# Optimization experiments

Measured on AMD Instinct MI355X. Metric: run time of the kernel, lower is better.

## Reference

```python
import jax, jax.numpy as jnp
import numpy as np


def _disk_samples(size):
    # Same construction as the torch module: regular grid on [-1,1]^2, keep points in unit disk.
    xs, ys = [], []
    for i in range(size):
        for j in range(size):
            x = i * 2.0 / (size - 1) - 1.0
            y = j * 2.0 / (size - 1) - 1.0
            if x * x + y * y <= 1.0:
                xs.append(x)
                ys.append(y)
    return np.asarray(xs, np.float32), np.asarray(ys, np.float32)


def setup_inputs() -> dict:
    key = jax.random.key(0)
    k1, k2, k3, k4, k5 = jax.random.split(key, 5)
    B, L, C, H, W = 1, 12, 3, 640, 640
    images = jax.random.uniform(k1, (B, L, C, H, W), dtype=jnp.float32)
    alphas = jax.random.uniform(k2, (B, L, 1, H, W), dtype=jnp.float32)
    coffs = jax.random.uniform(k3, (B, L, 1, H, W), dtype=jnp.float32)  # per-plane disparity-like map in [0,1)
    K = jax.random.uniform(k4, (B, 1, 1, 1), dtype=jnp.float32) * 20.0 + 2.0  # aperture radius in pixels
    depth_focus = jax.random.uniform(k5, (B, 1, 1, 1), dtype=jnp.float32)  # focus value, same units as coffs
    return {"images": images, "alphas": alphas, "coffs": coffs, "K": K,
            "depth_focus": depth_focus, "samples_per_side": 5}


def reference(images, alphas, coffs, K, depth_focus, samples_per_side):
    # Depth-aware ray-traced bokeh over an MPI stack.
    # For each output pixel and each circular aperture sample (u,v), gather from each
    # plane at an offset proportional to the plane's signed defocus radius
    #   r = K * (coff - depth_focus)
    # (nearest-pixel gather, clamped), then composite planes front-to-back with alpha,
    # and average over aperture samples.
    B, L, C, H, W = images.shape
    xs_np, ys_np = _disk_samples(int(samples_per_side))
    n_samples = len(xs_np)

    Kb = K[:, 0, 0, 0]                      # [B]
    df = depth_focus[:, 0, 0, 0]            # [B]
    coff = coffs[:, :, 0]                   # [B,L,H,W]
    r = Kb[:, None, None, None] * (coff - df[:, None, None, None])  # signed radius per plane/pixel

    a_flat = alphas[:, :, 0].reshape(B, L, H * W)       # [B,L,HW]
    img_flat = images.reshape(B, L, C, H * W)           # [B,L,C,HW]
    yy, xx = jnp.meshgrid(jnp.arange(H, dtype=jnp.float32),
                          jnp.arange(W, dtype=jnp.float32), indexing="ij")

    acc = jnp.zeros((B, C, H, W), images.dtype)
    for s in range(n_samples):  # small fixed aperture-sample set (static)
        qx = jnp.clip(jnp.round(xx + xs_np[s] * r), 0, W - 1).astype(jnp.int32)
        qy = jnp.clip(jnp.round(yy + ys_np[s] * r), 0, H - 1).astype(jnp.int32)
        idx = (qy * W + qx).reshape(B, L, H * W)
        a = jnp.take_along_axis(a_flat, idx, axis=2)                 # [B,L,HW]
        c = jnp.take_along_axis(img_flat, idx[:, :, None, :], axis=3)  # [B,L,C,HW]
        trans = jnp.cumprod(1.0 - a, axis=1)
        excl = jnp.concatenate([jnp.ones_like(a[:, :1]), trans[:, :-1]], axis=1)
        w = a * excl                                                  # front-to-back weights
        acc = acc + (w[:, :, None, :] * c).sum(axis=1).reshape(B, C, H, W)
    return acc / jnp.float32(n_samples)
```

## Files before the change

kernel.cpp:

```cpp
#include <hip/hip_runtime.h>

#define L_ 12
#define C_ 3
#define H_ 640
#define W_ 640
#define HW_ (H_*W_)

#define TS 40
#define HALO 22
#define LD (TS + 2*HALO)
#define NSLOT (LD*LD)
#define NT 1024
#define SIZE 5
#define NSAMP 13

__global__ __launch_bounds__(1024, 4) void render_tiled(
    const float* __restrict__ images,
    const float* __restrict__ alphas,
    const float* __restrict__ coffs,
    const float* __restrict__ Kp,
    const float* __restrict__ dfp,
    float* __restrict__ out) {
  __shared__ float4 tile[NSLOT];

  const int tid = threadIdx.x;
  const int tx0 = (int)(blockIdx.x % (W_ / TS)) * TS;
  const int ty0 = (int)(blockIdx.x / (W_ / TS)) * TS;
  const int bx0 = tx0 - HALO;
  const int by0 = ty0 - HALO;

  const float Kv = Kp[0];
  const float df = dfp[0];

  const int p0 = tid;
  const bool has2 = (tid < TS * TS - NT);
  const int p1 = tid + NT;

  const int x0 = tx0 + (p0 % TS), y0 = ty0 + (p0 / TS);
  const int x1 = tx0 + (p1 % TS), y1 = ty0 + (p1 / TS);
  const float xf0 = (float)x0, yf0 = (float)y0;
  const float xf1 = (float)x1, yf1 = (float)y1;

  float T0[NSAMP], T1[NSAMP];
#pragma unroll
  for (int s = 0; s < NSAMP; ++s) { T0[s] = 1.f; T1[s] = 1.f; }
  float a00 = 0.f, a01 = 0.f, a02 = 0.f;
  float a10 = 0.f, a11 = 0.f, a12 = 0.f;

  for (int l = 0; l < L_; ++l) {
    __syncthreads();
    const float* __restrict__ aP  = alphas + (size_t)l * HW_;
    const float* __restrict__ c0P = images + (size_t)(l * 3 + 0) * HW_;
    const float* __restrict__ c1P = images + (size_t)(l * 3 + 1) * HW_;
    const float* __restrict__ c2P = images + (size_t)(l * 3 + 2) * HW_;
    for (int s = tid; s < NSLOT; s += NT) {
      int hy = s / LD, hx = s - hy * LD;
      int gy = min(max(by0 + hy, 0), H_ - 1);
      int gx = min(max(bx0 + hx, 0), W_ - 1);
      int g = gy * W_ + gx;
      tile[s] = make_float4(aP[g], c0P[g], c1P[g], c2P[g]);
    }
    __syncthreads();

    const float r0 = __fmul_rn(Kv, __fsub_rn(coffs[(size_t)l * HW_ + y0 * W_ + x0], df));
    const float r1 = has2 ? __fmul_rn(Kv, __fsub_rn(coffs[(size_t)l * HW_ + y1 * W_ + x1], df)) : 0.f;

    int ord = 0;
#pragma unroll
    for (int i = 0; i < SIZE; ++i) {
#pragma unroll
      for (int j = 0; j < SIZE; ++j) {
        const double dx = (double)i * 2.0 / (SIZE - 1) - 1.0;
        const double dy = (double)j * 2.0 / (SIZE - 1) - 1.0;
        if (dx * dx + dy * dy <= 1.0) {
          const float sx = (float)dx;
          const float sy = (float)dy;
          {
            float qxf = rintf(__fadd_rn(xf0, __fmul_rn(sx, r0)));
            float qyf = rintf(__fadd_rn(yf0, __fmul_rn(sy, r0)));
            qxf = fminf(fmaxf(qxf, 0.f), (float)(W_ - 1));
            qyf = fminf(fmaxf(qyf, 0.f), (float)(H_ - 1));
            int idx = ((int)qyf - by0) * LD + ((int)qxf - bx0);
            float4 v = tile[idx];
            float w = v.x * T0[ord];
            a00 = __fmaf_rn(w, v.y, a00);
            a01 = __fmaf_rn(w, v.z, a01);
            a02 = __fmaf_rn(w, v.w, a02);
            T0[ord] *= (1.f - v.x);
          }
          if (has2) {
            float qxf = rintf(__fadd_rn(xf1, __fmul_rn(sx, r1)));
            float qyf = rintf(__fadd_rn(yf1, __fmul_rn(sy, r1)));
            qxf = fminf(fmaxf(qxf, 0.f), (float)(W_ - 1));
            qyf = fminf(fmaxf(qyf, 0.f), (float)(H_ - 1));
            int idx = ((int)qyf - by0) * LD + ((int)qxf - bx0);
            float4 v = tile[idx];
            float w = v.x * T1[ord];
            a10 = __fmaf_rn(w, v.y, a10);
            a11 = __fmaf_rn(w, v.z, a11);
            a12 = __fmaf_rn(w, v.w, a12);
            T1[ord] *= (1.f - v.x);
          }
          ++ord;
        }
      }
    }
  }

  const float inv_n_num = (float)NSAMP;
  {
    int g = y0 * W_ + x0;
    out[0 * HW_ + g] = a00 / inv_n_num;
    out[1 * HW_ + g] = a01 / inv_n_num;
    out[2 * HW_ + g] = a02 / inv_n_num;
  }
  if (has2) {
    int g = y1 * W_ + x1;
    out[0 * HW_ + g] = a10 / inv_n_num;
    out[1 * HW_ + g] = a11 / inv_n_num;
    out[2 * HW_ + g] = a12 / inv_n_num;
  }
}

extern "C" void kernel_launch(void* const* d_in, const int* in_sizes, int n_in,
                              void* d_out, int out_size, void* d_ws, size_t ws_size,
                              hipStream_t stream) {
  const float* images = (const float*)d_in[0];
  const float* alphas = (const float*)d_in[1];
  const float* coffs  = (const float*)d_in[2];
  const float* Kp     = (const float*)d_in[3];
  const float* dfp    = (const float*)d_in[4];
  float* out = (float*)d_out;

  const int tiles = (W_ / TS) * (H_ / TS);
  render_tiled<<<dim3(tiles), dim3(NT), 0, stream>>>(
      images, alphas, coffs, Kp, dfp, out);
}
```

Measured before the change: 179.0 us.

## Prefetch next plane's halo tile into registers while compositing current plane

Gather indices for the halo tile are computed once and kept in registers. Each plane's alpha and colour values are loaded into registers during compositing of the previous plane, then written to shared memory, so global latency overlaps with compute. Rounding and clamping work is skipped for aperture samples with a zero x or y offset. The cost is much higher register use (28 prefetch floats plus 7 indices per thread) at 1024 threads per block, which risks spills or lower occupancy.

```diff
diff --git a/kernel.cpp b/kernel.cpp
--- a/kernel.cpp
+++ b/kernel.cpp
@@ -1,7 +1,6 @@
 #include <hip/hip_runtime.h>
 
 #define L_ 12
-#define C_ 3
 #define H_ 640
 #define W_ 640
 #define HW_ (H_*W_)
@@ -11,10 +10,11 @@
 #define LD (TS + 2*HALO)
 #define NSLOT (LD*LD)
 #define NT 1024
+#define NSPT 7
 #define SIZE 5
 #define NSAMP 13
 
-__global__ __launch_bounds__(1024, 4) void render_tiled(
+__global__ __launch_bounds__(NT, 4) void render_tiled(
     const float* __restrict__ images,
     const float* __restrict__ alphas,
     const float* __restrict__ coffs,
@@ -32,14 +32,43 @@
   const float Kv = Kp[0];
   const float df = dfp[0];
 
-  const int p0 = tid;
   const bool has2 = (tid < TS * TS - NT);
   const int p1 = tid + NT;
 
-  const int x0 = tx0 + (p0 % TS), y0 = ty0 + (p0 / TS);
+  const int x0 = tx0 + (tid % TS), y0 = ty0 + (tid / TS);
   const int x1 = tx0 + (p1 % TS), y1 = ty0 + (p1 / TS);
   const float xf0 = (float)x0, yf0 = (float)y0;
   const float xf1 = (float)x1, yf1 = (float)y1;
+  const int rowbase0 = (y0 - by0) * LD, colbase0 = x0 - bx0;
+  const int rowbase1 = (y1 - by0) * LD, colbase1 = x1 - bx0;
+  const int src0 = y0 * W_ + x0;
+  const int src1 = y1 * W_ + x1;
+
+  int gidx[NSPT];
+#pragma unroll
+  for (int k = 0; k < NSPT; ++k) {
+    int s = tid + k * NT;
+    if (k < NSLOT / NT || s < NSLOT) {
+      int hy = s / LD, hx = s - hy * LD;
+      int gy = min(max(by0 + hy, 0), H_ - 1);
+      int gx = min(max(bx0 + hx, 0), W_ - 1);
+      gidx[k] = gy * W_ + gx;
+    }
+  }
+
+  float sa[NSPT], sc0[NSPT], sc1[NSPT], sc2[NSPT];
+#pragma unroll
+  for (int k = 0; k < NSPT; ++k) {
+    int s = tid + k * NT;
+    if (k < NSLOT / NT || s < NSLOT) {
+      sa[k]  = alphas[gidx[k]];
+      sc0[k] = images[(size_t)0 * HW_ + gidx[k]];
+      sc1[k] = images[(size_t)1 * HW_ + gidx[k]];
+      sc2[k] = images[(size_t)2 * HW_ + gidx[k]];
+    }
+  }
+  float cf0 = coffs[src0];
+  float cf1 = has2 ? coffs[src1] : 0.f;
 
   float T0[NSAMP], T1[NSAMP];
 #pragma unroll
@@ -49,21 +78,36 @@
 
   for (int l = 0; l < L_; ++l) {
     __syncthreads();
-    const float* __restrict__ aP  = alphas + (size_t)l * HW_;
-    const float* __restrict__ c0P = images + (size_t)(l * 3 + 0) * HW_;
-    const float* __restrict__ c1P = images + (size_t)(l * 3 + 1) * HW_;
-    const float* __restrict__ c2P = images + (size_t)(l * 3 + 2) * HW_;
-    for (int s = tid; s < NSLOT; s += NT) {
-      int hy = s / LD, hx = s - hy * LD;
-      int gy = min(max(by0 + hy, 0), H_ - 1);
-      int gx = min(max(bx0 + hx, 0), W_ - 1);
-      int g = gy * W_ + gx;
-      tile[s] = make_float4(aP[g], c0P[g], c1P[g], c2P[g]);
+#pragma unroll
+    for (int k = 0; k < NSPT; ++k) {
+      int s = tid + k * NT;
+      if (k < NSLOT / NT || s < NSLOT)
+        tile[s] = make_float4(sa[k], sc0[k], sc1[k], sc2[k]);
     }
     __syncthreads();
 
-    const float r0 = __fmul_rn(Kv, __fsub_rn(coffs[(size_t)l * HW_ + y0 * W_ + x0], df));
-    const float r1 = has2 ? __fmul_rn(Kv, __fsub_rn(coffs[(size_t)l * HW_ + y1 * W_ + x1], df)) : 0.f;
+    float ncf0 = 0.f, ncf1 = 0.f;
+    if (l + 1 < L_) {
+      const float* __restrict__ aP  = alphas + (size_t)(l + 1) * HW_;
+      const float* __restrict__ c0P = images + (size_t)((l + 1) * 3 + 0) * HW_;
+      const float* __restrict__ c1P = images + (size_t)((l + 1) * 3 + 1) * HW_;
+      const float* __restrict__ c2P = images + (size_t)((l + 1) * 3 + 2) * HW_;
+#pragma unroll
+      for (int k = 0; k < NSPT; ++k) {
+        int s = tid + k * NT;
+        if (k < NSLOT / NT || s < NSLOT) {
+          sa[k]  = aP[gidx[k]];
+          sc0[k] = c0P[gidx[k]];
+          sc1[k] = c1P[gidx[k]];
+          sc2[k] = c2P[gidx[k]];
+        }
+      }
+      ncf0 = coffs[(size_t)(l + 1) * HW_ + src0];
+      if (has2) ncf1 = coffs[(size_t)(l + 1) * HW_ + src1];
+    }
+
+    const float r0 = __fmul_rn(Kv, __fsub_rn(cf0, df));
+    const float r1 = __fmul_rn(Kv, __fsub_rn(cf1, df));
 
     int ord = 0;
 #pragma unroll
@@ -76,12 +120,22 @@
           const float sx = (float)dx;
           const float sy = (float)dy;
           {
-            float qxf = rintf(__fadd_rn(xf0, __fmul_rn(sx, r0)));
-            float qyf = rintf(__fadd_rn(yf0, __fmul_rn(sy, r0)));
-            qxf = fminf(fmaxf(qxf, 0.f), (float)(W_ - 1));
-            qyf = fminf(fmaxf(qyf, 0.f), (float)(H_ - 1));
-            int idx = ((int)qyf - by0) * LD + ((int)qxf - bx0);
-            float4 v = tile[idx];
+            int cx, ro;
+            if (dx == 0.0) {
+              cx = colbase0;
+            } else {
+              float qxf = rintf(__fadd_rn(xf0, __fmul_rn(sx, r0)));
+              qxf = fminf(fmaxf(qxf, 0.f), (float)(W_ - 1));
+              cx = (int)qxf - bx0;
+            }
+            if (dy == 0.0) {
+              ro = rowbase0;
+            } else {
+              float qyf = rintf(__fadd_rn(yf0, __fmul_rn(sy, r0)));
+              qyf = fminf(fmaxf(qyf, 0.f), (float)(H_ - 1));
+              ro = ((int)qyf - by0) * LD;
+            }
+            float4 v = tile[ro + cx];
             float w = v.x * T0[ord];
             a00 = __fmaf_rn(w, v.y, a00);
             a01 = __fmaf_rn(w, v.z, a01);
@@ -89,12 +143,22 @@
             T0[ord] *= (1.f - v.x);
           }
           if (has2) {
-            float qxf = rintf(__fadd_rn(xf1, __fmul_rn(sx, r1)));
-            float qyf = rintf(__fadd_rn(yf1, __fmul_rn(sy, r1)));
-            qxf = fminf(fmaxf(qxf, 0.f), (float)(W_ - 1));
-            qyf = fminf(fmaxf(qyf, 0.f), (float)(H_ - 1));
-            int idx = ((int)qyf - by0) * LD + ((int)qxf - bx0);
-            float4 v = tile[idx];
+            int cx, ro;
+            if (dx == 0.0) {
+              cx = colbase1;
+            } else {
+              float qxf = rintf(__fadd_rn(xf1, __fmul_rn(sx, r1)));
+              qxf = fminf(fmaxf(qxf, 0.f), (float)(W_ - 1));
+              cx = (int)qxf - bx0;
+            }
+            if (dy == 0.0) {
+              ro = rowbase1;
+            } else {
+              float qyf = rintf(__fadd_rn(yf1, __fmul_rn(sy, r1)));
+              qyf = fminf(fmaxf(qyf, 0.f), (float)(H_ - 1));
+              ro = ((int)qyf - by0) * LD;
+            }
+            float4 v = tile[ro + cx];
             float w = v.x * T1[ord];
             a10 = __fmaf_rn(w, v.y, a10);
             a11 = __fmaf_rn(w, v.z, a11);
@@ -105,20 +169,18 @@
         }
       }
     }
-  }
-
-  const float inv_n_num = (float)NSAMP;
-  {
-    int g = y0 * W_ + x0;
-    out[0 * HW_ + g] = a00 / inv_n_num;
-    out[1 * HW_ + g] = a01 / inv_n_num;
-    out[2 * HW_ + g] = a02 / inv_n_num;
-  }
+    cf0 = ncf0;
+    cf1 = ncf1;
+  }
+
+  const float n = (float)NSAMP;
+  out[0 * HW_ + src0] = a00 / n;
+  out[1 * HW_ + src0] = a01 / n;
+  out[2 * HW_ + src0] = a02 / n;
   if (has2) {
-    int g = y1 * W_ + x1;
-    out[0 * HW_ + g] = a10 / inv_n_num;
-    out[1 * HW_ + g] = a11 / inv_n_num;
-    out[2 * HW_ + g] = a12 / inv_n_num;
+    out[0 * HW_ + src1] = a10 / n;
+    out[1 * HW_ + src1] = a11 / n;
+    out[2 * HW_ + src1] = a12 / n;
   }
 }
 
```

Result: slower. 286.2 us (+59.9%).
